# Performance work log

Measured on AMD Instinct MI355X. Metric: run time of the kernel, lower is better.

The kernel has to match this reference:

```python
import jax, jax.numpy as jnp
import numpy as np

B, T, C = 2, 2048, 2048
N, K, H = 16, 4, 128      # heads, kv heads, head dim
G = N // K                # query groups per kv head
ROPE_THETA = 10000.0
N_LAYERS = 24
SOFTCAP = 50.0


def _sine_table(features, length, max_timescale):
    fraction = jnp.arange(0, features, 2, dtype=jnp.float32) / features
    timescale = max_timescale ** fraction  # min_timescale = 1.0
    sinusoid = jnp.einsum('i,j->ij', jnp.arange(length, dtype=jnp.float32),
                          1.0 / timescale, precision=jax.lax.Precision.HIGHEST)
    sinusoid = jnp.concatenate([sinusoid, sinusoid], axis=-1)  # (length, features)
    return jnp.sin(sinusoid), jnp.cos(sinusoid)


def _rotate_half(x):
    x1, x2 = jnp.split(x, 2, axis=-1)
    return jnp.concatenate([-x2, x1], axis=-1)


def setup_inputs() -> dict:
    key = jax.random.key(0)
    kx, kq, kk, kv, ko = jax.random.split(key, 5)
    init_std = np.sqrt(2.0 / (5.0 * C)).astype(np.float32)
    wang_std = np.float32(2.0 / N_LAYERS / np.sqrt(N * H))
    return {
        'x': jax.random.normal(kx, (B, T, C), dtype=jnp.float32),
        'q_kernel': jax.random.normal(kq, (C, N * H), dtype=jnp.float32) * init_std,
        'k_kernel': jax.random.normal(kk, (C, K * H), dtype=jnp.float32) * init_std,
        'v_kernel': jax.random.normal(kv, (C, K * H), dtype=jnp.float32) * init_std,
        'out_kernel': jax.random.normal(ko, (N * H, C), dtype=jnp.float32) * wang_std,
    }


def reference(x, q_kernel, k_kernel, v_kernel, out_kernel):
    q = jnp.dot(x, q_kernel).reshape(B, T, K, G, H)
    k = jnp.dot(x, k_kernel).reshape(B, T, K, H)
    v = jnp.dot(x, v_kernel).reshape(B, T, K, H)

    # RoPE (note original passes cos into the `sin` slot and vice versa by name,
    # but the computation uses cos with identity part and sin with rotate_half).
    sin, cos = _sine_table(H, T, ROPE_THETA)
    qcos = cos[None, :, None, None, :]  # (1,T,1,1,H)
    qsin = sin[None, :, None, None, :]
    kcos = cos[None, :, None, :]        # (1,T,1,H)
    ksin = sin[None, :, None, :]
    q = q * qcos + _rotate_half(q) * qsin
    k = k * kcos + _rotate_half(k) * ksin

    scale = jax.lax.rsqrt(jnp.float32(H))
    logits = jnp.einsum('btkgh,bskh->bkgts', q * scale, k)  # (B,K,G,T,S)
    logits = jnp.tanh(logits / SOFTCAP) * SOFTCAP
    causal = jnp.tril(jnp.ones((T, T), dtype=jnp.bool_))
    neg = jnp.asarray(-0.7 * jnp.finfo(logits.dtype).max, dtype=logits.dtype)
    logits = jnp.where(causal[None, None, None, :, :], logits, neg)
    probs = jax.nn.softmax(logits.astype(jnp.float32), axis=-1).astype(logits.dtype)
    encoded = jnp.einsum('bkgts,bskh->btkgh', probs, v)
    encoded = encoded.reshape(B, T, N * H)
    return jnp.dot(encoded, out_kernel)
```

## Files before the change

### kernel.cpp

```cpp
#include <hip/hip_runtime.h>
#include <stdint.h>

typedef unsigned short u16;
typedef __bf16 bf16x8 __attribute__((ext_vector_type(8)));
typedef __bf16 bf16x4 __attribute__((ext_vector_type(4)));
typedef float f32x4 __attribute__((ext_vector_type(4)));

#define T_SEQ 2048
#define KVH 4

__device__ __forceinline__ u16 f2b(float f) {
  uint32_t u = __builtin_bit_cast(uint32_t, f);
  u += 0x7FFFu + ((u >> 16) & 1u);
  return (u16)(u >> 16);
}
__device__ __forceinline__ float b2f(u16 h) {
  uint32_t u = ((uint32_t)h) << 16;
  return __builtin_bit_cast(float, u);
}

__device__ __forceinline__ void gload16(const void* g, void* l) {
  __builtin_amdgcn_global_load_lds((const __attribute__((address_space(1))) void*)g,
                                   (__attribute__((address_space(3))) void*)l, 16, 0, 0);
}

__global__ void k_f32_to_bf16(const float* __restrict__ in, u16* __restrict__ out, int n4) {
  int i = blockIdx.x * blockDim.x + threadIdx.x;
  if (i >= n4) return;
  float4 v = reinterpret_cast<const float4*>(in)[i];
  ushort4 o;
  o.x = f2b(v.x); o.y = f2b(v.y); o.z = f2b(v.z); o.w = f2b(v.w);
  reinterpret_cast<ushort4*>(out)[i] = o;
}

__global__ void k_transpose_all(const float* __restrict__ wq, const float* __restrict__ wk,
                                const float* __restrict__ wv, const float* __restrict__ wo,
                                u16* __restrict__ wqkvt, u16* __restrict__ wot) {
  __shared__ float tile[32][33];
  const int z = blockIdx.z;
  int bx = blockIdx.x;
  const float* in;
  u16* out;
  int Cc;
  if (z == 0)      { in = wq; out = wqkvt;              Cc = 2048; }
  else if (z == 1) { in = wo; out = wot;                Cc = 2048; }
  else {
    if (bx < 16)      { in = wk; out = wqkvt + 2048 * 2048; Cc = 512; }
    else if (bx < 32) { in = wv; out = wqkvt + 2560 * 2048; Cc = 512; bx -= 16; }
    else return;
  }
  const int R = 2048;
  const int c0 = bx * 32, r0 = blockIdx.y * 32;
  const int tx = threadIdx.x, ty = threadIdx.y;
  for (int i = ty; i < 32; i += 8) tile[i][tx] = in[(size_t)(r0 + i) * Cc + c0 + tx];
  __syncthreads();
  for (int i = ty; i < 32; i += 8) out[(size_t)(c0 + i) * R + r0 + tx] = f2b(tile[tx][i]);
}

template <int OUT_BF16>
__global__ __launch_bounds__(256, 3) void k_gemm(const u16* __restrict__ A,
                                                 const u16* __restrict__ Bt,
                                                 void* __restrict__ Cp,
                                                 int M, int N, int Kd,
                                                 int lda, int ldb, int ldc) {
  __align__(16) __shared__ u16 As[128 * 32];
  __align__(16) __shared__ u16 Bs[128 * 32];
  const int tid = threadIdx.x;
  const int wid = tid >> 6, lane = tid & 63;
  const int lg = lane >> 4, lm = lane & 15;
  const int nwg = gridDim.x * gridDim.y;
  int f = blockIdx.y * gridDim.x + blockIdx.x;
  f = (f & 7) * (nwg >> 3) + (f >> 3);
  const int bm = f % gridDim.x, bn = f / gridDim.x;
  const int wr = wid >> 1, wc = wid & 1;

  const int srow = wid * 32 + (lane >> 2);
  const int scol = (lane & 3) * 8;
  const u16* ap0 = A + (size_t)(bm * 128 + srow) * lda + scol;
  const u16* ap1 = ap0 + (size_t)16 * lda;
  const u16* bp0 = Bt + (size_t)(bn * 128 + srow) * ldb + scol;
  const u16* bp1 = bp0 + (size_t)16 * ldb;
  u16* asDst0 = As + wid * 1024;
  u16* asDst1 = As + wid * 1024 + 512;
  u16* bsDst0 = Bs + wid * 1024;
  u16* bsDst1 = Bs + wid * 1024 + 512;

  const f32x4 z4 = {0.f, 0.f, 0.f, 0.f};
  f32x4 acc[4][4];
#pragma unroll
  for (int i = 0; i < 4; ++i)
#pragma unroll
    for (int j = 0; j < 4; ++j) acc[i][j] = z4;

  const int nk = Kd >> 5;
  for (int kb = 0; kb < nk; ++kb) {
    gload16(ap0, asDst0);
    gload16(ap1, asDst1);
    gload16(bp0, bsDst0);
    gload16(bp1, bsDst1);
    ap0 += 32; ap1 += 32; bp0 += 32; bp1 += 32;
    __syncthreads();
    bf16x8 af[4], bfr[4];
#pragma unroll
    for (int i = 0; i < 4; ++i)
      af[i] = *(const bf16x8*)(As + (wr * 64 + i * 16 + lm) * 32 + lg * 8);
#pragma unroll
    for (int j = 0; j < 4; ++j)
      bfr[j] = *(const bf16x8*)(Bs + (wc * 64 + j * 16 + lm) * 32 + lg * 8);
#pragma unroll
    for (int i = 0; i < 4; ++i)
#pragma unroll
      for (int j = 0; j < 4; ++j)
        acc[i][j] = __builtin_amdgcn_mfma_f32_16x16x32_bf16(af[i], bfr[j], acc[i][j], 0, 0, 0);
    __syncthreads();
  }

#pragma unroll
  for (int i = 0; i < 4; ++i) {
    const int row = bm * 128 + wr * 64 + i * 16 + lg * 4;
#pragma unroll
    for (int j = 0; j < 4; ++j) {
      const int col = bn * 128 + wc * 64 + j * 16 + lm;
#pragma unroll
      for (int r = 0; r < 4; ++r) {
        const float v = acc[i][j][r];
        if (OUT_BF16)
          ((u16*)Cp)[(size_t)(row + r) * ldc + col] = __builtin_bit_cast(u16, (__bf16)v);
        else
          ((float*)Cp)[(size_t)(row + r) * ldc + col] = v;
      }
    }
  }
}

__global__ void k_rope_v(const u16* __restrict__ qkv, u16* __restrict__ kbf,
                         u16* __restrict__ vt) {
  __shared__ u16 tile[32][33];
  const int bid = blockIdx.x;
  const int tid = threadIdx.x;
  if (bid < 4096) {
    const int idx = bid * 256 + tid;
    const int j = idx & 63;
    const int kh = (idx >> 6) & 3;
    const int m = idx >> 8;
    const int t = m & (T_SEQ - 1);
    const int b = m >> 11;
    const float inv = __expf((float)j * -0.14391157f);
    const float ang = (float)t * inv;
    float s, c;
    __sincosf(ang, &s, &c);
    const u16* row = qkv + (size_t)m * 3072 + 2048 + kh * 128;
    const float x1 = b2f(row[j]), x2 = b2f(row[j + 64]);
    u16* orow = kbf + ((size_t)(b * KVH + kh) * T_SEQ + t) * 128;
    orow[j] = f2b(x1 * c - x2 * s);
    orow[j + 64] = f2b(x2 * c + x1 * s);
  } else {
    const int vb = bid - 4096;
    const int t0 = (vb & 63) * 32, h0 = ((vb >> 6) & 3) * 32, bk = vb >> 8;
    const int b = bk >> 2, kh = bk & 3;
    const int tx = tid & 31, ty = tid >> 5;
    for (int i = ty; i < 32; i += 8)
      tile[i][tx] = qkv[(size_t)(b * T_SEQ + t0 + i) * 3072 + 2560 + kh * 128 + h0 + tx];
    __syncthreads();
    for (int i = ty; i < 32; i += 8)
      vt[(size_t)bk * (128 * T_SEQ) + (size_t)(h0 + i) * T_SEQ + t0 + tx] = tile[tx][i];
  }
}

__global__ __launch_bounds__(256, 2) void k_attn(const u16* __restrict__ qkv,
                                                 const u16* __restrict__ kbf,
                                                 const u16* __restrict__ vt,
                                                 u16* __restrict__ enc) {
  __shared__ __align__(16) u16 smem[36864];
  u16* const Ks0 = smem;
  u16* const Vs0 = smem + 16384;

  const int n = blockIdx.y, b = blockIdx.z;
  const int qt = (b == 0) ? (15 - blockIdx.x) : blockIdx.x;
  const int kh = n >> 2;
  const int tid = threadIdx.x;
  const int wid = tid >> 6;
  const int lane = tid & 63;
  const int lg = lane >> 4;
  const int lm = lane & 15;
  const int q0w = qt * 128 + wid * 32;
  u16* const Pl = smem + 32768 + wid * 1024;

  bf16x8 qfA[4], qfB[4];
  {
    const u16* qa = qkv + (size_t)(b * T_SEQ + q0w + lm) * 3072 + n * 128 + lg * 8;
    const u16* qb_ = qa + 16 * 3072;
    bf16x8 ra[4], rb[4];
#pragma unroll
    for (int c = 0; c < 4; ++c) {
      ra[c] = *(const bf16x8*)(qa + c * 32);
      rb[c] = *(const bf16x8*)(qb_ + c * 32);
    }
    const float scale = 0.08838834764831845f;
    const float tA = (float)(q0w + lm), tB = (float)(q0w + 16 + lm);
#pragma unroll
    for (int c = 0; c < 2; ++c) {
#pragma unroll
      for (int k = 0; k < 8; ++k) {
        const float inv = __expf((float)(c * 32 + lg * 8 + k) * -0.14391157f);
        float sA, cA, sB, cB;
        __sincosf(tA * inv, &sA, &cA);
        __sincosf(tB * inv, &sB, &cB);
        const float a1 = (float)ra[c][k], a2 = (float)ra[c + 2][k];
        const float b1 = (float)rb[c][k], b2 = (float)rb[c + 2][k];
        qfA[c][k]     = (__bf16)((a1 * cA - a2 * sA) * scale);
        qfA[c + 2][k] = (__bf16)((a2 * cA + a1 * sA) * scale);
        qfB[c][k]     = (__bf16)((b1 * cB - b2 * sB) * scale);
        qfB[c + 2][k] = (__bf16)((b2 * cB + b1 * sB) * scale);
      }
    }
  }
  const u16* const kg = kbf + (size_t)(b * KVH + kh) * T_SEQ * 128;
  const u16* const vg = vt + (size_t)(b * KVH + kh) * 128 * T_SEQ;

  const int swz = lm & 7;
  int koff[4], voff[2], poff[4];
#pragma unroll
  for (int c = 0; c < 4; ++c) koff[c] = lm * 128 + (((c * 4 + lg) ^ swz) * 8);
#pragma unroll
  for (int ks = 0; ks < 2; ++ks) voff[ks] = lm * 64 + (((ks * 4 + lg) ^ swz) * 8);
#pragma unroll
  for (int st = 0; st < 4; ++st)
    poff[st] = lm * 64 + (((st * 2 + (lg >> 1)) ^ swz) * 8) + (lg & 1) * 4;

  const f32x4 z4 = {0.f, 0.f, 0.f, 0.f};
  f32x4 accA[8], accB[8];
#pragma unroll
  for (int h = 0; h < 8; ++h) { accA[h] = z4; accB[h] = z4; }
  float lA = 0.f, lB = 0.f;

  const int ntiles = 2 * qt + 2;

  auto STAGE = [&](int buf, int kb2) {
    const int kv2 = kb2 * 64;
    const u16* ksrc = kg + (size_t)kv2 * 128;
    u16* kdst = Ks0 + buf * 8192;
    u16* vdst = Vs0 + buf * 8192;
#pragma unroll
    for (int i = 0; i < 4; ++i) {
      const int g = tid + i * 256;
      const int row = g >> 4, u = g & 15;
      gload16(ksrc + row * 128 + ((u ^ (row & 7)) * 8), kdst + g * 8);
    }
#pragma unroll
    for (int i = 0; i < 4; ++i) {
      const int g = tid + i * 256;
      const int row = g >> 3, u = g & 7;
      gload16(vg + (size_t)row * T_SEQ + kv2 + ((u ^ (row & 7)) * 8), vdst + g * 8);
    }
  };

  auto tile_pc = [&](f32x4* sa, float* p, float& lsum, int tg, bool needMask, int kv) {
#pragma unroll
    for (int st = 0; st < 4; ++st)
#pragma unroll
      for (int r = 0; r < 4; ++r) p[st * 4 + r] = sa[st][r];
#pragma unroll
    for (int i = 0; i < 16; ++i) {
      const float e = __builtin_amdgcn_exp2f(p[i] * 0.05770780163555853f);
      p[i] = __builtin_amdgcn_exp2f(-144.269504088896f * __builtin_amdgcn_rcpf(e + 1.f));
    }
    if (needMask) {
#pragma unroll
      for (int i = 0; i < 16; ++i) {
        const int sg = kv + (i >> 2) * 16 + lg * 4 + (i & 3);
        if (sg > tg) p[i] = 0.f;
      }
    }
#pragma unroll
    for (int i = 0; i < 16; ++i) lsum += p[i];
  };
  auto tile_pw = [&](const float* p) {
#pragma unroll
    for (int st = 0; st < 4; ++st) {
      bf16x4 w4;
#pragma unroll
      for (int r = 0; r < 4; ++r) w4[r] = (__bf16)p[st * 4 + r];
      *(bf16x4*)(Pl + poff[st]) = w4;
    }
  };

  STAGE(0, 0);
  asm volatile("s_waitcnt vmcnt(0)" ::: "memory");
  __syncthreads();

  for (int kb = 0; kb < ntiles; ++kb) {
    const int cur = kb & 1;
    if (kb + 1 < ntiles) STAGE(cur ^ 1, kb + 1);
    const int kv = kb * 64;
    if (kv <= q0w + 31) {
      const u16* KsC = Ks0 + cur * 8192;
      const u16* VsC = Vs0 + cur * 8192;

      f32x4 saA[4] = {z4, z4, z4, z4};
      f32x4 saB[4] = {z4, z4, z4, z4};
      __builtin_amdgcn_s_setprio(1);
#pragma unroll
      for (int st = 0; st < 4; ++st) {
#pragma unroll
        for (int c = 0; c < 4; ++c) {
          const bf16x8 kf = *(const bf16x8*)(KsC + st * 2048 + koff[c]);
          saA[st] = __builtin_amdgcn_mfma_f32_16x16x32_bf16(kf, qfA[c], saA[st], 0, 0, 0);
          saB[st] = __builtin_amdgcn_mfma_f32_16x16x32_bf16(kf, qfB[c], saB[st], 0, 0, 0);
        }
      }
      __builtin_amdgcn_s_setprio(0);

      float pA[16], pB[16];
      tile_pc(saA, pA, lA, q0w + lm, kv + 63 > q0w, kv);
      tile_pw(pA);
      tile_pc(saB, pB, lB, q0w + 16 + lm, kv + 63 > q0w + 16, kv);
      asm volatile("s_waitcnt lgkmcnt(0)" ::: "memory");
      bf16x8 pfA[2], pfB[2];
#pragma unroll
      for (int ks = 0; ks < 2; ++ks) pfA[ks] = *(const bf16x8*)(Pl + voff[ks]);
      tile_pw(pB);
      asm volatile("s_waitcnt lgkmcnt(0)" ::: "memory");
#pragma unroll
      for (int ks = 0; ks < 2; ++ks) pfB[ks] = *(const bf16x8*)(Pl + voff[ks]);

      __builtin_amdgcn_s_setprio(1);
#pragma unroll
      for (int h = 0; h < 8; ++h) {
#pragma unroll
        for (int ks = 0; ks < 2; ++ks) {
          const bf16x8 vf = *(const bf16x8*)(VsC + h * 1024 + voff[ks]);
          accA[h] = __builtin_amdgcn_mfma_f32_16x16x32_bf16(pfA[ks], vf, accA[h], 0, 0, 0);
          accB[h] = __builtin_amdgcn_mfma_f32_16x16x32_bf16(pfB[ks], vf, accB[h], 0, 0, 0);
        }
      }
      __builtin_amdgcn_s_setprio(0);
    }
    asm volatile("s_waitcnt vmcnt(0)" ::: "memory");
    __syncthreads();
  }

  lA += __shfl_xor(lA, 16); lA += __shfl_xor(lA, 32);
  lB += __shfl_xor(lB, 16); lB += __shfl_xor(lB, 32);
  float liA[4], liB[4];
#pragma unroll
  for (int r = 0; r < 4; ++r) {
    liA[r] = 1.f / __shfl(lA, lg * 4 + r);
    liB[r] = 1.f / __shfl(lB, lg * 4 + r);
  }
#pragma unroll
  for (int h = 0; h < 8; ++h) {
#pragma unroll
    for (int r = 0; r < 4; ++r) {
      const size_t colo = n * 128 + h * 16 + lm;
      enc[(size_t)(b * T_SEQ + q0w + lg * 4 + r) * 2048 + colo] =
          __builtin_bit_cast(u16, (__bf16)(accA[h][r] * liA[r]));
      enc[(size_t)(b * T_SEQ + q0w + 16 + lg * 4 + r) * 2048 + colo] =
          __builtin_bit_cast(u16, (__bf16)(accB[h][r] * liB[r]));
    }
  }
}

extern "C" void kernel_launch(void* const* d_in, const int* in_sizes, int n_in,
                              void* d_out, int out_size, void* d_ws, size_t ws_size,
                              hipStream_t stream) {
  const float* x  = (const float*)d_in[0];
  const float* wq = (const float*)d_in[1];
  const float* wk = (const float*)d_in[2];
  const float* wv = (const float*)d_in[3];
  const float* wo = (const float*)d_in[4];

  char* ws = (char*)d_ws;
  u16* x_bf  = (u16*)(ws);
  u16* wqkvt = (u16*)(ws + 16777216);
  u16* wot   = (u16*)(ws + 29360128);
  u16* qkv   = (u16*)(ws + 37748736);
  u16* enc   = (u16*)(ws + 62914560);
  u16* k_bf  = (u16*)(ws + 79691776);
  u16* vt    = (u16*)(ws + 83886080);
  if (ws_size < 88080384) return;
  (void)in_sizes; (void)n_in; (void)out_size;

  k_f32_to_bf16<<<dim3(8192), dim3(256), 0, stream>>>(x, x_bf, 8388608 / 4);
  k_transpose_all<<<dim3(64, 64, 3), dim3(32, 8), 0, stream>>>(wq, wk, wv, wo, wqkvt, wot);
  k_gemm<1><<<dim3(32, 24), dim3(256), 0, stream>>>(x_bf, wqkvt, qkv,
                                                    4096, 3072, 2048, 2048, 2048, 3072);
  k_rope_v<<<dim3(6144), dim3(256), 0, stream>>>(qkv, k_bf, vt);
  k_attn<<<dim3(16, 16, 2), dim3(256), 0, stream>>>(qkv, k_bf, vt, enc);
  k_gemm<0><<<dim3(32, 16), dim3(256), 0, stream>>>(enc, wot, d_out,
                                                    4096, 2048, 2048, 2048, 2048, 2048);
}
```

Baseline: 204.2 us.

## Double GEMM K-tile with XOR-swizzled LDS and fuse prep kernels

```diff
diff --git a/kernel.cpp b/kernel.cpp
--- a/kernel.cpp
+++ b/kernel.cpp
@@ -24,20 +24,25 @@
                                    (__attribute__((address_space(3))) void*)l, 16, 0, 0);
 }
 
-__global__ void k_f32_to_bf16(const float* __restrict__ in, u16* __restrict__ out, int n4) {
-  int i = blockIdx.x * blockDim.x + threadIdx.x;
-  if (i >= n4) return;
-  float4 v = reinterpret_cast<const float4*>(in)[i];
-  ushort4 o;
-  o.x = f2b(v.x); o.y = f2b(v.y); o.z = f2b(v.z); o.w = f2b(v.w);
-  reinterpret_cast<ushort4*>(out)[i] = o;
-}
-
-__global__ void k_transpose_all(const float* __restrict__ wq, const float* __restrict__ wk,
-                                const float* __restrict__ wv, const float* __restrict__ wo,
-                                u16* __restrict__ wqkvt, u16* __restrict__ wot) {
+__global__ void k_prep(const float* __restrict__ x, u16* __restrict__ x_bf,
+                       const float* __restrict__ wq, const float* __restrict__ wk,
+                       const float* __restrict__ wv, const float* __restrict__ wo,
+                       u16* __restrict__ wqkvt, u16* __restrict__ wot) {
+  const int z = blockIdx.z;
+  const int tid = threadIdx.y * 32 + threadIdx.x;
+  if (z == 3) {
+    const int base = (blockIdx.y * 64 + blockIdx.x) * 256 + tid;
+#pragma unroll
+    for (int rep = 0; rep < 2; ++rep) {
+      const int i = base + rep * 1048576;
+      float4 v = reinterpret_cast<const float4*>(x)[i];
+      ushort4 o;
+      o.x = f2b(v.x); o.y = f2b(v.y); o.z = f2b(v.z); o.w = f2b(v.w);
+      reinterpret_cast<ushort4*>(x_bf)[i] = o;
+    }
+    return;
+  }
   __shared__ float tile[32][33];
-  const int z = blockIdx.z;
   int bx = blockIdx.x;
   const float* in;
   u16* out;
@@ -63,8 +68,8 @@
                                                  void* __restrict__ Cp,
                                                  int M, int N, int Kd,
                                                  int lda, int ldb, int ldc) {
-  __align__(16) __shared__ u16 As[128 * 32];
-  __align__(16) __shared__ u16 Bs[128 * 32];
+  __align__(16) __shared__ u16 As[128 * 64];
+  __align__(16) __shared__ u16 Bs[128 * 64];
   const int tid = threadIdx.x;
   const int wid = tid >> 6, lane = tid & 63;
   const int lg = lane >> 4, lm = lane & 15;
@@ -74,16 +79,25 @@
   const int bm = f % gridDim.x, bn = f / gridDim.x;
   const int wr = wid >> 1, wc = wid & 1;
 
-  const int srow = wid * 32 + (lane >> 2);
-  const int scol = (lane & 3) * 8;
-  const u16* ap0 = A + (size_t)(bm * 128 + srow) * lda + scol;
-  const u16* ap1 = ap0 + (size_t)16 * lda;
-  const u16* bp0 = Bt + (size_t)(bn * 128 + srow) * ldb + scol;
-  const u16* bp1 = bp0 + (size_t)16 * ldb;
-  u16* asDst0 = As + wid * 1024;
-  u16* asDst1 = As + wid * 1024 + 512;
-  u16* bsDst0 = Bs + wid * 1024;
-  u16* bsDst1 = Bs + wid * 1024 + 512;
+  const u16* ap[4];
+  const u16* bp[4];
+#pragma unroll
+  for (int i = 0; i < 4; ++i) {
+    const int g = tid + i * 256;
+    const int row = g >> 3, u = g & 7;
+    ap[i] = A + (size_t)(bm * 128 + row) * lda + ((u ^ (row & 7)) * 8);
+    bp[i] = Bt + (size_t)(bn * 128 + row) * ldb + ((u ^ (row & 7)) * 8);
+  }
+
+  const int swzl = lm & 7;
+  int aoff[4][2], boff[4][2];
+#pragma unroll
+  for (int i = 0; i < 4; ++i)
+#pragma unroll
+    for (int kk = 0; kk < 2; ++kk) {
+      aoff[i][kk] = (wr * 64 + i * 16 + lm) * 64 + (((kk * 4 + lg) ^ swzl) * 8);
+      boff[i][kk] = (wc * 64 + i * 16 + lm) * 64 + (((kk * 4 + lg) ^ swzl) * 8);
+    }
 
   const f32x4 z4 = {0.f, 0.f, 0.f, 0.f};
   f32x4 acc[4][4];
@@ -92,26 +106,31 @@
 #pragma unroll
     for (int j = 0; j < 4; ++j) acc[i][j] = z4;
 
-  const int nk = Kd >> 5;
+  const int nk = Kd >> 6;
   for (int kb = 0; kb < nk; ++kb) {
-    gload16(ap0, asDst0);
-    gload16(ap1, asDst1);
-    gload16(bp0, bsDst0);
-    gload16(bp1, bsDst1);
-    ap0 += 32; ap1 += 32; bp0 += 32; bp1 += 32;
+#pragma unroll
+    for (int i = 0; i < 4; ++i) {
+      const int g = tid + i * 256;
+      gload16(ap[i], As + g * 8);
+      gload16(bp[i], Bs + g * 8);
+      ap[i] += 64;
+      bp[i] += 64;
+    }
     __syncthreads();
-    bf16x8 af[4], bfr[4];
-#pragma unroll
-    for (int i = 0; i < 4; ++i)
-      af[i] = *(const bf16x8*)(As + (wr * 64 + i * 16 + lm) * 32 + lg * 8);
-#pragma unroll
-    for (int j = 0; j < 4; ++j)
-      bfr[j] = *(const bf16x8*)(Bs + (wc * 64 + j * 16 + lm) * 32 + lg * 8);
-#pragma unroll
-    for (int i = 0; i < 4; ++i)
-#pragma unroll
-      for (int j = 0; j < 4; ++j)
-        acc[i][j] = __builtin_amdgcn_mfma_f32_16x16x32_bf16(af[i], bfr[j], acc[i][j], 0, 0, 0);
+#pragma unroll
+    for (int kk = 0; kk < 2; ++kk) {
+      bf16x8 af[4], bfr[4];
+#pragma unroll
+      for (int i = 0; i < 4; ++i) {
+        af[i] = *(const bf16x8*)(As + aoff[i][kk]);
+        bfr[i] = *(const bf16x8*)(Bs + boff[i][kk]);
+      }
+#pragma unroll
+      for (int i = 0; i < 4; ++i)
+#pragma unroll
+        for (int j = 0; j < 4; ++j)
+          acc[i][j] = __builtin_amdgcn_mfma_f32_16x16x32_bf16(af[i], bfr[j], acc[i][j], 0, 0, 0);
+    }
     __syncthreads();
   }
 
@@ -381,8 +400,7 @@
   if (ws_size < 88080384) return;
   (void)in_sizes; (void)n_in; (void)out_size;
 
-  k_f32_to_bf16<<<dim3(8192), dim3(256), 0, stream>>>(x, x_bf, 8388608 / 4);
-  k_transpose_all<<<dim3(64, 64, 3), dim3(32, 8), 0, stream>>>(wq, wk, wv, wo, wqkvt, wot);
+  k_prep<<<dim3(64, 64, 4), dim3(32, 8), 0, stream>>>(x, x_bf, wq, wk, wv, wo, wqkvt, wot);
   k_gemm<1><<<dim3(32, 24), dim3(256), 0, stream>>>(x_bf, wqkvt, qkv,
                                                     4096, 3072, 2048, 2048, 2048, 3072);
   k_rope_v<<<dim3(6144), dim3(256), 0, stream>>>(qkv, k_bf, vt);
```

Result: faster. 187.4 us, median of 3 (-8.2%).
